# Kernel tuning notes

Hardware: AMD Instinct MI355X
Metric: run time of the kernel (lower is better)

## Reference

```python
import jax, jax.numpy as jnp
import numpy as np

N = 128       # n_channels
B = 131072    # batch
C = np.float32(np.sqrt(0.5))  # 50/50 beamsplitter amplitude (c = s = sqrt(0.5))


def setup_inputs() -> dict:
    key = jax.random.key(0)
    k1, k2, k3, k4 = jax.random.split(key, 4)
    M = N * (N - 1) // 2
    return {
        "x_real": jax.random.normal(k1, (B, N), jnp.float32),
        "x_imag": jax.random.normal(k2, (B, N), jnp.float32),
        "mzi_phases": jax.random.normal(k3, (M * 2,), jnp.float32) * 0.1,
        "output_phases": jax.random.normal(k4, (N,), jnp.float32) * 0.1,
    }


def _construct_unitary(mzi_phases, output_phases):
    n = output_phases.shape[0]
    m = n * (n - 1) // 2
    # pair ordering matches the torch double loop: i ascending, then j > i (row-major triu)
    i_np, j_np = np.triu_indices(n, 1)
    i_idx = jnp.asarray(i_np, jnp.int32)
    j_idx = jnp.asarray(j_np, jnp.int32)
    ph = mzi_phases.reshape(m, 2)
    theta, phi = ph[:, 0], ph[:, 1]

    def step(U, xs):
        th, ph_, i, j = xs
        e_phi = jax.lax.complex(jnp.cos(ph_), jnp.sin(ph_))
        e_th = jax.lax.complex(jnp.cos(th), jnp.sin(th))
        ri = U[i]
        rj = U[j]
        # T_ij @ U touches only rows i and j (O(N) Givens row update)
        new_i = C * ri + (C * e_phi) * rj
        new_j = (C * e_th) * ri - (C * e_th * e_phi) * rj
        U = U.at[i].set(new_i).at[j].set(new_j)
        return U, None

    def chunk_body(U, xs_chunk):
        U, _ = jax.lax.scan(step, U, xs_chunk)
        return U, None

    # chunk the M sequential updates: M = (n-1) * (n//2) for even n;
    # checkpointing chunks keeps reverse-mode memory O(sqrt-ish) instead of O(M * N^2)
    n_chunks = n - 1
    cs = n // 2
    xs = (theta.reshape(n_chunks, cs), phi.reshape(n_chunks, cs),
          i_idx.reshape(n_chunks, cs), j_idx.reshape(n_chunks, cs))
    U0 = jnp.eye(n, dtype=jnp.complex64)
    U, _ = jax.lax.scan(jax.checkpoint(chunk_body), U0, xs)
    # output phase screen D @ U
    d = jax.lax.complex(jnp.cos(output_phases), jnp.sin(output_phases))
    return d[:, None] * U


def reference(x_real, x_imag, mzi_phases, output_phases):
    U = _construct_unitary(mzi_phases, output_phases)           # [N, N] complex64
    x = jax.lax.complex(x_real, x_imag)                          # [B, N] complex64
    # matmul(U, x.unsqueeze(-1)).squeeze(-1) == x @ U^T
    out = jnp.einsum('nm,bm->bn', U, x)                          # [B, N] complex64
    # ComplexDropout is identity in eval mode
    return out
```

## Files before the change

kernel.cpp:

```cpp
#include <hip/hip_runtime.h>
#include <hip/hip_bf16.h>

#define NDIM 128
#define N2   (NDIM * NDIM)
#define BDIM 131072
#define NMZI 8128
#define NCHUNK 16
#define NJG 8
#define NCOL 32
#define NLOC 16
static constexpr float CC = 0.70710678118654752440f;

typedef __attribute__((ext_vector_type(8))) short bf16x8;
typedef __attribute__((ext_vector_type(4))) float f32x4;

__device__ __align__(16) float2         g_V[NCHUNK * N2];
__device__ __align__(16) float2         g_W[4 * N2];
__device__ __align__(16) unsigned short g_TB[32 * NDIM * 8];
__device__ __align__(16) unsigned short g_Ur[16 * NDIM * 8];
__device__ __align__(16) unsigned short g_Ui[16 * NDIM * 8];

__device__ inline unsigned short f2bf(float f) {
    union { __hip_bfloat16 h; unsigned short u; } cv;
    cv.h = __float2bfloat16(f);
    return cv.u;
}

#define CFMA(acc, av, b)                                                    \
    acc.x = fmaf(av.x, b.x, fmaf(-av.y, b.y, acc.x));                       \
    acc.y = fmaf(av.x, b.y, fmaf( av.y, b.x, acc.y));

__global__ __launch_bounds__(256) void build_scan(const float* __restrict__ mzi) {
    __shared__ float2 Usm[NDIM][NCOL];
    __shared__ float4 ph[2][NDIM];
    __shared__ float4 cmp[NJG][NCOL];
    const int tid   = threadIdx.x;
    const int c     = tid & 31;
    const int g     = tid >> 5;
    const int col0  = blockIdx.x * NCOL;
    const int chunk = blockIdx.y;
    const int i0    = chunk * 8;
    const int iEnd  = min(i0 + 8, NDIM - 1);
    const int nsw   = iEnd - i0;

    for (int k = g; k < NDIM; k += NJG)
        Usm[k][c] = make_float2((k == col0 + c) ? 1.f : 0.f, 0.f);

    const float2* mzp = (const float2*)mzi;
    int base = 127 * i0 - (i0 * (i0 - 1)) / 2;
    {
        const int L0 = NDIM - 1 - i0;
        if (tid < L0) {
            const float2 mz = mzp[base + tid];
            float sp, cp, st, ct;
            sincosf(mz.y, &sp, &cp);
            sincosf(mz.x, &st, &ct);
            ph[0][tid] = make_float4(cp, sp, CC * ct, CC * st);
        }
    }
    __syncthreads();

    #pragma unroll 1
    for (int sw = 0; sw < nsw; ++sw) {
        const int i = i0 + sw;
        const int L = NDIM - 1 - i;
        const int cur = sw & 1;

        float2 mznext;
        const bool have = (sw < nsw - 1) && (tid < L - 1);
        if (have) mznext = mzp[base + L + tid];

        const float2 r0 = Usm[i][c];
        const int nloc  = (L + NJG - 1) >> 3;
        const int myBeg = g * nloc;
        const int myN   = max(0, min(nloc, L - myBeg));

        float2 treg[NLOC];
        float2 qth[NLOC];
        float  A = 1.f;
        float2 Bc = make_float2(0.f, 0.f);
        #pragma unroll
        for (int kk = 0; kk < NLOC; ++kk) {
            if (kk < myN) {
                const int off = myBeg + kk;
                const float4 q  = ph[cur][off];
                const float2 rj = Usm[i + 1 + off][c];
                const float tr = fmaf(q.x, rj.x, -q.y * rj.y);
                const float ti = fmaf(q.x, rj.y,  q.y * rj.x);
                treg[kk] = make_float2(tr, ti);
                qth[kk]  = make_float2(q.z, q.w);
                Bc.x = CC * (Bc.x + tr);
                Bc.y = CC * (Bc.y + ti);
                A *= CC;
            }
        }
        cmp[g][c] = make_float4(A, Bc.x, Bc.y, 0.f);
        __syncthreads();

        float2 r = r0;
        for (int h2 = 0; h2 < g; ++h2) {
            const float4 cm = cmp[h2][c];
            r.x = fmaf(cm.x, r.x, cm.y);
            r.y = fmaf(cm.x, r.y, cm.z);
        }

        #pragma unroll
        for (int kk = 0; kk < NLOC; ++kk) {
            if (kk < myN) {
                const float2 t = treg[kk];
                const float2 q = qth[kk];
                const float dr = r.x - t.x, di = r.y - t.y;
                const float njx = fmaf(q.x, dr, -q.y * di);
                const float njy = fmaf(q.x, di,  q.y * dr);
                Usm[i + 1 + myBeg + kk][c] = make_float2(njx, njy);
                r.x = CC * (r.x + t.x);
                r.y = CC * (r.y + t.y);
            }
        }
        if (myN > 0 && (myBeg + myN == L))
            Usm[i][c] = r;

        if (have) {
            float sp, cp, st, ct;
            sincosf(mznext.y, &sp, &cp);
            sincosf(mznext.x, &st, &ct);
            ph[cur ^ 1][tid] = make_float4(cp, sp, CC * ct, CC * st);
        }
        __syncthreads();
        base += L;
    }

    float2* Vp = g_V + chunk * N2;
    for (int k = g; k < NDIM; k += NJG)
        Vp[k * NDIM + col0 + c] = Usm[k][c];
}

__global__ __launch_bounds__(256) void compose_quad() {
    __shared__ float2 As[4 * NDIM];
    __shared__ float2 part[2][4][NDIM];
    const int tid = threadIdx.x;
    const int h   = tid >> 7;
    const int m   = tid & 127;
    const int gq  = blockIdx.y;
    const int n0  = blockIdx.x * 4;

    if (h == 0) {
        const float2* A = g_V + (4 * gq + 3) * N2;
        #pragma unroll
        for (int r = 0; r < 4; ++r) As[r * NDIM + m] = A[(n0 + r) * NDIM + m];
    }
    __syncthreads();

    #pragma unroll 1
    for (int step = 2; step >= 0; --step) {
        const float2* B = g_V + (4 * gq + step) * N2;
        const int kbase = h * 64;
        float2 a0 = {0.f, 0.f}, a1 = {0.f, 0.f}, a2 = {0.f, 0.f}, a3 = {0.f, 0.f};
        float2 bb[8];
        #pragma unroll
        for (int u = 0; u < 8; ++u) bb[u] = B[(kbase + u) * NDIM + m];
        #pragma unroll 1
        for (int k0 = 0; k0 < 64; k0 += 8) {
            #pragma unroll
            for (int u = 0; u < 8; ++u) {
                const float2 bv = bb[u];
                bb[u] = B[(kbase + k0 + 8 + u) * NDIM + m];
                const int k = kbase + k0 + u;
                float2 av;
                av = As[0 * NDIM + k]; CFMA(a0, av, bv)
                av = As[1 * NDIM + k]; CFMA(a1, av, bv)
                av = As[2 * NDIM + k]; CFMA(a2, av, bv)
                av = As[3 * NDIM + k]; CFMA(a3, av, bv)
            }
        }
        part[h][0][m] = a0; part[h][1][m] = a1;
        part[h][2][m] = a2; part[h][3][m] = a3;
        __syncthreads();
        if (h == 0) {
            #pragma unroll
            for (int r = 0; r < 4; ++r) {
                const float2 p0 = part[0][r][m], p1 = part[1][r][m];
                const float2 s = make_float2(p0.x + p1.x, p0.y + p1.y);
                if (step > 0) As[r * NDIM + m] = s;
                else          g_W[gq * N2 + (n0 + r) * NDIM + m] = s;
            }
        }
        __syncthreads();
    }
}

__global__ __launch_bounds__(256) void compose_final4(const float* __restrict__ oph) {
    __shared__ float2 As[4 * NDIM];
    __shared__ float2 part[2][4][NDIM];
    const int tid = threadIdx.x;
    const int h   = tid >> 7;
    const int m   = tid & 127;
    const int n0  = blockIdx.x * 4;

    if (h == 0) {
        const float2* A = g_W + 3 * N2;
        #pragma unroll
        for (int r = 0; r < 4; ++r) As[r * NDIM + m] = A[(n0 + r) * NDIM + m];
    }
    __syncthreads();

    #pragma unroll 1
    for (int step = 2; step >= 0; --step) {
        const float2* B = g_W + step * N2;
        const int kbase = h * 64;
        float2 a0 = {0.f, 0.f}, a1 = {0.f, 0.f}, a2 = {0.f, 0.f}, a3 = {0.f, 0.f};
        float2 bb[8];
        #pragma unroll
        for (int u = 0; u < 8; ++u) bb[u] = B[(kbase + u) * NDIM + m];
        #pragma unroll 1
        for (int k0 = 0; k0 < 64; k0 += 8) {
            #pragma unroll
            for (int u = 0; u < 8; ++u) {
                const float2 bv = bb[u];
                bb[u] = B[(kbase + k0 + 8 + u) * NDIM + m];
                const int k = kbase + k0 + u;
                float2 av;
                av = As[0 * NDIM + k]; CFMA(a0, av, bv)
                av = As[1 * NDIM + k]; CFMA(a1, av, bv)
                av = As[2 * NDIM + k]; CFMA(a2, av, bv)
                av = As[3 * NDIM + k]; CFMA(a3, av, bv)
            }
        }
        part[h][0][m] = a0; part[h][1][m] = a1;
        part[h][2][m] = a2; part[h][3][m] = a3;
        __syncthreads();
        if (h == 0) {
            if (step > 0) {
                #pragma unroll
                for (int r = 0; r < 4; ++r) {
                    const float2 p0 = part[0][r][m], p1 = part[1][r][m];
                    As[r * NDIM + m] = make_float2(p0.x + p1.x, p0.y + p1.y);
                }
            } else {
                const int kg = m >> 3, e = m & 7;
                #pragma unroll
                for (int r = 0; r < 4; ++r) {
                    const float2 p0 = part[0][r][m], p1 = part[1][r][m];
                    const float2 u = make_float2(p0.x + p1.x, p0.y + p1.y);
                    const int n = n0 + r;
                    float ds, dc;
                    sincosf(oph[n], &ds, &dc);
                    const float vr = fmaf(u.x, dc, -u.y * ds);
                    const float vi = fmaf(u.x, ds,  u.y * dc);
                    g_TB[(kg * NDIM + n) * 8 + e]        = f2bf(vr);
                    g_TB[((16 + kg) * NDIM + n) * 8 + e] = f2bf(-vi);
                    g_Ur[(kg * NDIM + n) * 8 + e] = f2bf(vr);
                    g_Ui[(kg * NDIM + n) * 8 + e] = f2bf(vi);
                }
            }
        }
        __syncthreads();
    }
}

__global__ __launch_bounds__(256) void cmatmul0(const float* __restrict__ xr,
                                                const float* __restrict__ xi,
                                                float* __restrict__ out) {
    __shared__ __align__(16) char smX[4][8192];
    const int tid  = threadIdx.x;
    const int lane = tid & 63;
    const int w    = tid >> 6;
    const int r15  = lane & 15;
    const int kg4  = lane >> 4;
    const int l31  = lane & 31;
    const int lh   = lane >> 5;
    const int R    = blockIdx.x * 64 + w * 16;

    const f32x4* sre = (const f32x4*)(xr + (size_t)R * NDIM);
    const f32x4* sim = (const f32x4*)(xi + (size_t)R * NDIM);
    f32x4 G[16];
    #pragma unroll
    for (int p = 0; p < 8; ++p) G[p]     = __builtin_nontemporal_load(sre + p * 64 + lane);
    #pragma unroll
    for (int p = 0; p < 8; ++p) G[8 + p] = __builtin_nontemporal_load(sim + p * 64 + lane);

    char* buf = &smX[w][0];
    #pragma unroll
    for (int p = 0; p < 8; ++p) {
        const int row = 2 * p + lh;
        const int swz = (row & 7) << 4;
        uint2 v;
        v.x = ((unsigned)f2bf(G[p][1]) << 16) | f2bf(G[p][0]);
        v.y = ((unsigned)f2bf(G[p][3]) << 16) | f2bf(G[p][2]);
        *(uint2*)(buf + row * 512 + ((l31 * 8) ^ swz)) = v;
        v.x = ((unsigned)f2bf(G[8 + p][1]) << 16) | f2bf(G[8 + p][0]);
        v.y = ((unsigned)f2bf(G[8 + p][3]) << 16) | f2bf(G[8 + p][2]);
        *(uint2*)(buf + row * 512 + 256 + ((l31 * 8) ^ swz)) = v;
    }

    bf16x8 fx[8];
    const int rswz = (r15 & 7) << 4;
    #pragma unroll
    for (int kc = 0; kc < 8; ++kc) {
        const int off = (((kc & 3) * 64 + kg4 * 16) ^ rswz) + ((kc >= 4) ? 256 : 0);
        fx[kc] = *(const bf16x8*)(buf + r15 * 512 + off);
    }

    const bf16x8* gT = (const bf16x8*)g_TB;
    #pragma unroll
    for (int nt = 0; nt < 8; ++nt) {
        f32x4 a0 = {0.f, 0.f, 0.f, 0.f};
        f32x4 a1 = {0.f, 0.f, 0.f, 0.f};
        #pragma unroll
        for (int kc = 0; kc < 4; ++kc)
            a0 = __builtin_amdgcn_mfma_f32_16x16x32_bf16(
                gT[(kc * 4 + kg4) * NDIM + nt * 16 + r15], fx[kc], a0, 0, 0, 0);
        #pragma unroll
        for (int kc = 4; kc < 8; ++kc)
            a1 = __builtin_amdgcn_mfma_f32_16x16x32_bf16(
                gT[(kc * 4 + kg4) * NDIM + nt * 16 + r15], fx[kc], a1, 0, 0, 0);
        const f32x4 s = a0 + a1;
        *(f32x4*)(buf + r15 * 512 + ((nt * 64 + kg4 * 16) ^ rswz)) = s;
    }

    char* outp = (char*)(out + (size_t)R * NDIM);
    #pragma unroll
    for (int p = 0; p < 8; ++p) {
        const int bofs = p * 1024 + lane * 16;
        const int row  = bofs >> 9;
        const int colb = bofs & 511;
        const f32x4 v = *(const f32x4*)(buf + row * 512 + (colb ^ ((row & 7) << 4)));
        __builtin_nontemporal_store(v, (f32x4*)(outp + bofs));
    }
}

__global__ __launch_bounds__(256) void cmatmul1(const float* __restrict__ xr,
                                                const float* __restrict__ xi,
                                                ushort2* __restrict__ outp) {
    const int lane  = threadIdx.x & 63;
    const int w     = threadIdx.x >> 6;
    const int btile = blockIdx.x * 64 + w * 16;
    const int r15   = lane & 15;
    const int kg4   = lane >> 4;
    const int bload = btile + r15;

    const bf16x8* Ur = (const bf16x8*)g_Ur;
    const bf16x8* Ui = (const bf16x8*)g_Ui;
    const float* xrp = xr + (size_t)bload * NDIM;
    const float* xip = xi + (size_t)bload * NDIM;

    bf16x8 ar[4], ai[4], ain[4];
    #pragma unroll
    for (int kc = 0; kc < 4; ++kc) {
        const int k0 = kc * 32 + kg4 * 8;
        float4 rlo = *(const float4*)(xrp + k0);
        float4 rhi = *(const float4*)(xrp + k0 + 4);
        float4 ilo = *(const float4*)(xip + k0);
        float4 ihi = *(const float4*)(xip + k0 + 4);
        bf16x8 vr, vi, vn;
        vr[0] = (short)f2bf(rlo.x); vr[1] = (short)f2bf(rlo.y);
        vr[2] = (short)f2bf(rlo.z); vr[3] = (short)f2bf(rlo.w);
        vr[4] = (short)f2bf(rhi.x); vr[5] = (short)f2bf(rhi.y);
        vr[6] = (short)f2bf(rhi.z); vr[7] = (short)f2bf(rhi.w);
        vi[0] = (short)f2bf(ilo.x); vi[1] = (short)f2bf(ilo.y);
        vi[2] = (short)f2bf(ilo.z); vi[3] = (short)f2bf(ilo.w);
        vi[4] = (short)f2bf(ihi.x); vi[5] = (short)f2bf(ihi.y);
        vi[6] = (short)f2bf(ihi.z); vi[7] = (short)f2bf(ihi.w);
        #pragma unroll
        for (int e = 0; e < 8; ++e) vn[e] = (short)(vi[e] ^ 0x8000);
        ar[kc] = vr; ai[kc] = vi; ain[kc] = vn;
    }

    #pragma unroll
    for (int nt = 0; nt < 8; ++nt) {
        f32x4 accR = {0.f, 0.f, 0.f, 0.f};
        f32x4 accI = {0.f, 0.f, 0.f, 0.f};
        #pragma unroll
        for (int kc = 0; kc < 4; ++kc) {
            const int kg = kc * 4 + kg4;
            bf16x8 br = Ur[kg * NDIM + nt * 16 + r15];
            bf16x8 bi = Ui[kg * NDIM + nt * 16 + r15];
            accR = __builtin_amdgcn_mfma_f32_16x16x32_bf16(ar[kc],  br, accR, 0, 0, 0);
            accR = __builtin_amdgcn_mfma_f32_16x16x32_bf16(ain[kc], bi, accR, 0, 0, 0);
            accI = __builtin_amdgcn_mfma_f32_16x16x32_bf16(ar[kc],  bi, accI, 0, 0, 0);
            accI = __builtin_amdgcn_mfma_f32_16x16x32_bf16(ai[kc],  br, accI, 0, 0, 0);
        }
        const int n    = nt * 16 + r15;
        const int brow = btile + kg4 * 4;
        #pragma unroll
        for (int r = 0; r < 4; ++r)
            outp[(size_t)(brow + r) * NDIM + n] = make_ushort2(f2bf(accR[r]), f2bf(accI[r]));
    }
}

extern "C" void kernel_launch(void* const* d_in, const int* in_sizes, int n_in,
                              void* d_out, int out_size, void* d_ws, size_t ws_size,
                              hipStream_t stream) {
    const float* xr  = (const float*)d_in[0];
    const float* xi  = (const float*)d_in[1];
    const float* mzi = (const float*)d_in[2];
    const float* oph = (const float*)d_in[3];

    build_scan<<<dim3(4, NCHUNK), dim3(256), 0, stream>>>(mzi);
    compose_quad<<<dim3(32, 4), dim3(256), 0, stream>>>();
    compose_final4<<<dim3(32), dim3(256), 0, stream>>>(oph);
    if (out_size == BDIM * NDIM) {
        cmatmul0<<<dim3(BDIM / 64), dim3(256), 0, stream>>>(xr, xi, (float*)d_out);
    } else {
        cmatmul1<<<dim3(BDIM / 64), dim3(256), 0, stream>>>(xr, xi, (ushort2*)d_out);
    }
}
```

Before: 110.4 us.

## Fuse unitary build and compose kernels into one persistent kernel with grid barriers

Merges the three small build/compose kernels into one 128-block kernel, separated by atomic-counter grid barriers. The aim is to remove two kernel launch gaps from the critical path. The counters are reset at the start of the following matmul kernel, so correctness relies on all 128 blocks being co-resident and on that reset running before the next call. Blocks that have no scan work now sit idle waiting at the barrier.

```diff
diff --git a/kernel.cpp b/kernel.cpp
--- a/kernel.cpp
+++ b/kernel.cpp
@@ -6,6 +6,7 @@
 #define BDIM 131072
 #define NMZI 8128
 #define NCHUNK 16
+#define NBLK 128
 #define NJG 8
 #define NCOL 32
 #define NLOC 16
@@ -19,6 +20,7 @@
 __device__ __align__(16) unsigned short g_TB[32 * NDIM * 8];
 __device__ __align__(16) unsigned short g_Ur[16 * NDIM * 8];
 __device__ __align__(16) unsigned short g_Ui[16 * NDIM * 8];
+__device__ unsigned g_ctr[3];
 
 __device__ inline unsigned short f2bf(float f) {
     union { __hip_bfloat16 h; unsigned short u; } cv;
@@ -26,241 +28,271 @@
     return cv.u;
 }
 
+__device__ __forceinline__ void gbar(int idx) {
+    __syncthreads();
+    asm volatile("" ::: "memory");
+    if (threadIdx.x == 0) {
+        __threadfence();
+        __hip_atomic_fetch_add(&g_ctr[idx], 1u, __ATOMIC_RELEASE, __HIP_MEMORY_SCOPE_AGENT);
+        while (__hip_atomic_load(&g_ctr[idx], __ATOMIC_RELAXED, __HIP_MEMORY_SCOPE_AGENT)
+               < (unsigned)NBLK)
+            __builtin_amdgcn_s_sleep(2);
+        __threadfence();
+    }
+    __syncthreads();
+    asm volatile("" ::: "memory");
+}
+
 #define CFMA(acc, av, b)                                                    \
     acc.x = fmaf(av.x, b.x, fmaf(-av.y, b.y, acc.x));                       \
     acc.y = fmaf(av.x, b.y, fmaf( av.y, b.x, acc.y));
 
-__global__ __launch_bounds__(256) void build_scan(const float* __restrict__ mzi) {
-    __shared__ float2 Usm[NDIM][NCOL];
-    __shared__ float4 ph[2][NDIM];
-    __shared__ float4 cmp[NJG][NCOL];
-    const int tid   = threadIdx.x;
-    const int c     = tid & 31;
-    const int g     = tid >> 5;
-    const int col0  = blockIdx.x * NCOL;
-    const int chunk = blockIdx.y;
-    const int i0    = chunk * 8;
-    const int iEnd  = min(i0 + 8, NDIM - 1);
-    const int nsw   = iEnd - i0;
-
-    for (int k = g; k < NDIM; k += NJG)
-        Usm[k][c] = make_float2((k == col0 + c) ? 1.f : 0.f, 0.f);
-
-    const float2* mzp = (const float2*)mzi;
-    int base = 127 * i0 - (i0 * (i0 - 1)) / 2;
+__global__ __launch_bounds__(256) void build_all(const float* __restrict__ mzi,
+                                                 const float* __restrict__ oph) {
+    __shared__ __align__(16) char SM[40960];
+    const int tid = threadIdx.x;
+    const int b   = blockIdx.x;
+
+    if (b < 64) {
+        float2 (*Usm)[NCOL] = reinterpret_cast<float2(*)[NCOL]>(SM);
+        float4 (*ph)[NDIM]  = reinterpret_cast<float4(*)[NDIM]>(SM + 32768);
+        float4 (*cmp)[NCOL] = reinterpret_cast<float4(*)[NCOL]>(SM + 36864);
+        const int c     = tid & 31;
+        const int g     = tid >> 5;
+        const int col0  = (b & 3) * NCOL;
+        const int chunk = b >> 2;
+        const int i0    = chunk * 8;
+        const int iEnd  = min(i0 + 8, NDIM - 1);
+        const int nsw   = iEnd - i0;
+
+        for (int k = g; k < NDIM; k += NJG)
+            Usm[k][c] = make_float2((k == col0 + c) ? 1.f : 0.f, 0.f);
+
+        const float2* mzp = (const float2*)mzi;
+        int base = 127 * i0 - (i0 * (i0 - 1)) / 2;
+        {
+            const int L0 = NDIM - 1 - i0;
+            if (tid < L0) {
+                const float2 mz = mzp[base + tid];
+                float sp, cp, st, ct;
+                sincosf(mz.y, &sp, &cp);
+                sincosf(mz.x, &st, &ct);
+                ph[0][tid] = make_float4(cp, sp, CC * ct, CC * st);
+            }
+        }
+        __syncthreads();
+
+        #pragma unroll 1
+        for (int sw = 0; sw < nsw; ++sw) {
+            const int i = i0 + sw;
+            const int L = NDIM - 1 - i;
+            const int cur = sw & 1;
+
+            float2 mznext;
+            const bool have = (sw < nsw - 1) && (tid < L - 1);
+            if (have) mznext = mzp[base + L + tid];
+
+            const float2 r0 = Usm[i][c];
+            const int nloc  = (L + NJG - 1) >> 3;
+            const int myBeg = g * nloc;
+            const int myN   = max(0, min(nloc, L - myBeg));
+
+            float2 treg[NLOC];
+            float2 qth[NLOC];
+            float  A = 1.f;
+            float2 Bc = make_float2(0.f, 0.f);
+            #pragma unroll
+            for (int kk = 0; kk < NLOC; ++kk) {
+                if (kk < myN) {
+                    const int off = myBeg + kk;
+                    const float4 q  = ph[cur][off];
+                    const float2 rj = Usm[i + 1 + off][c];
+                    const float tr = fmaf(q.x, rj.x, -q.y * rj.y);
+                    const float ti = fmaf(q.x, rj.y,  q.y * rj.x);
+                    treg[kk] = make_float2(tr, ti);
+                    qth[kk]  = make_float2(q.z, q.w);
+                    Bc.x = CC * (Bc.x + tr);
+                    Bc.y = CC * (Bc.y + ti);
+                    A *= CC;
+                }
+            }
+            cmp[g][c] = make_float4(A, Bc.x, Bc.y, 0.f);
+            __syncthreads();
+
+            float2 r = r0;
+            for (int h2 = 0; h2 < g; ++h2) {
+                const float4 cm = cmp[h2][c];
+                r.x = fmaf(cm.x, r.x, cm.y);
+                r.y = fmaf(cm.x, r.y, cm.z);
+            }
+
+            #pragma unroll
+            for (int kk = 0; kk < NLOC; ++kk) {
+                if (kk < myN) {
+                    const float2 t = treg[kk];
+                    const float2 q = qth[kk];
+                    const float dr = r.x - t.x, di = r.y - t.y;
+                    const float njx = fmaf(q.x, dr, -q.y * di);
+                    const float njy = fmaf(q.x, di,  q.y * dr);
+                    Usm[i + 1 + myBeg + kk][c] = make_float2(njx, njy);
+                    r.x = CC * (r.x + t.x);
+                    r.y = CC * (r.y + t.y);
+                }
+            }
+            if (myN > 0 && (myBeg + myN == L))
+                Usm[i][c] = r;
+
+            if (have) {
+                float sp, cp, st, ct;
+                sincosf(mznext.y, &sp, &cp);
+                sincosf(mznext.x, &st, &ct);
+                ph[cur ^ 1][tid] = make_float4(cp, sp, CC * ct, CC * st);
+            }
+            __syncthreads();
+            base += L;
+        }
+
+        float2* Vp = g_V + chunk * N2;
+        for (int k = g; k < NDIM; k += NJG)
+            Vp[k * NDIM + col0 + c] = Usm[k][c];
+    }
+
+    gbar(0);
+
     {
-        const int L0 = NDIM - 1 - i0;
-        if (tid < L0) {
-            const float2 mz = mzp[base + tid];
-            float sp, cp, st, ct;
-            sincosf(mz.y, &sp, &cp);
-            sincosf(mz.x, &st, &ct);
-            ph[0][tid] = make_float4(cp, sp, CC * ct, CC * st);
-        }
-    }
-    __syncthreads();
-
-    #pragma unroll 1
-    for (int sw = 0; sw < nsw; ++sw) {
-        const int i = i0 + sw;
-        const int L = NDIM - 1 - i;
-        const int cur = sw & 1;
-
-        float2 mznext;
-        const bool have = (sw < nsw - 1) && (tid < L - 1);
-        if (have) mznext = mzp[base + L + tid];
-
-        const float2 r0 = Usm[i][c];
-        const int nloc  = (L + NJG - 1) >> 3;
-        const int myBeg = g * nloc;
-        const int myN   = max(0, min(nloc, L - myBeg));
-
-        float2 treg[NLOC];
-        float2 qth[NLOC];
-        float  A = 1.f;
-        float2 Bc = make_float2(0.f, 0.f);
-        #pragma unroll
-        for (int kk = 0; kk < NLOC; ++kk) {
-            if (kk < myN) {
-                const int off = myBeg + kk;
-                const float4 q  = ph[cur][off];
-                const float2 rj = Usm[i + 1 + off][c];
-                const float tr = fmaf(q.x, rj.x, -q.y * rj.y);
-                const float ti = fmaf(q.x, rj.y,  q.y * rj.x);
-                treg[kk] = make_float2(tr, ti);
-                qth[kk]  = make_float2(q.z, q.w);
-                Bc.x = CC * (Bc.x + tr);
-                Bc.y = CC * (Bc.y + ti);
-                A *= CC;
-            }
-        }
-        cmp[g][c] = make_float4(A, Bc.x, Bc.y, 0.f);
+        float2* As = (float2*)SM;
+        float2 (*part)[4][NDIM] =
+            reinterpret_cast<float2(*)[4][NDIM]>(SM + 4096);
+        const int h  = tid >> 7;
+        const int m  = tid & 127;
+        const int gq = b >> 5;
+        const int n0 = (b & 31) * 4;
+
+        if (h == 0) {
+            const float2* A = g_V + (4 * gq + 3) * N2;
+            #pragma unroll
+            for (int r = 0; r < 4; ++r) As[r * NDIM + m] = A[(n0 + r) * NDIM + m];
+        }
         __syncthreads();
 
-        float2 r = r0;
-        for (int h2 = 0; h2 < g; ++h2) {
-            const float4 cm = cmp[h2][c];
-            r.x = fmaf(cm.x, r.x, cm.y);
-            r.y = fmaf(cm.x, r.y, cm.z);
-        }
-
-        #pragma unroll
-        for (int kk = 0; kk < NLOC; ++kk) {
-            if (kk < myN) {
-                const float2 t = treg[kk];
-                const float2 q = qth[kk];
-                const float dr = r.x - t.x, di = r.y - t.y;
-                const float njx = fmaf(q.x, dr, -q.y * di);
-                const float njy = fmaf(q.x, di,  q.y * dr);
-                Usm[i + 1 + myBeg + kk][c] = make_float2(njx, njy);
-                r.x = CC * (r.x + t.x);
-                r.y = CC * (r.y + t.y);
-            }
-        }
-        if (myN > 0 && (myBeg + myN == L))
-            Usm[i][c] = r;
-
-        if (have) {
-            float sp, cp, st, ct;
-            sincosf(mznext.y, &sp, &cp);
-            sincosf(mznext.x, &st, &ct);
-            ph[cur ^ 1][tid] = make_float4(cp, sp, CC * ct, CC * st);
-        }
-        __syncthreads();
-        base += L;
-    }
-
-    float2* Vp = g_V + chunk * N2;
-    for (int k = g; k < NDIM; k += NJG)
-        Vp[k * NDIM + col0 + c] = Usm[k][c];
-}
-
-__global__ __launch_bounds__(256) void compose_quad() {
-    __shared__ float2 As[4 * NDIM];
-    __shared__ float2 part[2][4][NDIM];
-    const int tid = threadIdx.x;
-    const int h   = tid >> 7;
-    const int m   = tid & 127;
-    const int gq  = blockIdx.y;
-    const int n0  = blockIdx.x * 4;
-
-    if (h == 0) {
-        const float2* A = g_V + (4 * gq + 3) * N2;
-        #pragma unroll
-        for (int r = 0; r < 4; ++r) As[r * NDIM + m] = A[(n0 + r) * NDIM + m];
-    }
-    __syncthreads();
-
-    #pragma unroll 1
-    for (int step = 2; step >= 0; --step) {
-        const float2* B = g_V + (4 * gq + step) * N2;
-        const int kbase = h * 64;
-        float2 a0 = {0.f, 0.f}, a1 = {0.f, 0.f}, a2 = {0.f, 0.f}, a3 = {0.f, 0.f};
-        float2 bb[8];
-        #pragma unroll
-        for (int u = 0; u < 8; ++u) bb[u] = B[(kbase + u) * NDIM + m];
         #pragma unroll 1
-        for (int k0 = 0; k0 < 64; k0 += 8) {
-            #pragma unroll
-            for (int u = 0; u < 8; ++u) {
-                const float2 bv = bb[u];
-                bb[u] = B[(kbase + k0 + 8 + u) * NDIM + m];
-                const int k = kbase + k0 + u;
-                float2 av;
-                av = As[0 * NDIM + k]; CFMA(a0, av, bv)
-                av = As[1 * NDIM + k]; CFMA(a1, av, bv)
-                av = As[2 * NDIM + k]; CFMA(a2, av, bv)
-                av = As[3 * NDIM + k]; CFMA(a3, av, bv)
-            }
-        }
-        part[h][0][m] = a0; part[h][1][m] = a1;
-        part[h][2][m] = a2; part[h][3][m] = a3;
-        __syncthreads();
-        if (h == 0) {
-            #pragma unroll
-            for (int r = 0; r < 4; ++r) {
-                const float2 p0 = part[0][r][m], p1 = part[1][r][m];
-                const float2 s = make_float2(p0.x + p1.x, p0.y + p1.y);
-                if (step > 0) As[r * NDIM + m] = s;
-                else          g_W[gq * N2 + (n0 + r) * NDIM + m] = s;
-            }
-        }
-        __syncthreads();
-    }
-}
-
-__global__ __launch_bounds__(256) void compose_final4(const float* __restrict__ oph) {
-    __shared__ float2 As[4 * NDIM];
-    __shared__ float2 part[2][4][NDIM];
-    const int tid = threadIdx.x;
-    const int h   = tid >> 7;
-    const int m   = tid & 127;
-    const int n0  = blockIdx.x * 4;
-
-    if (h == 0) {
-        const float2* A = g_W + 3 * N2;
-        #pragma unroll
-        for (int r = 0; r < 4; ++r) As[r * NDIM + m] = A[(n0 + r) * NDIM + m];
-    }
-    __syncthreads();
-
-    #pragma unroll 1
-    for (int step = 2; step >= 0; --step) {
-        const float2* B = g_W + step * N2;
-        const int kbase = h * 64;
-        float2 a0 = {0.f, 0.f}, a1 = {0.f, 0.f}, a2 = {0.f, 0.f}, a3 = {0.f, 0.f};
-        float2 bb[8];
-        #pragma unroll
-        for (int u = 0; u < 8; ++u) bb[u] = B[(kbase + u) * NDIM + m];
-        #pragma unroll 1
-        for (int k0 = 0; k0 < 64; k0 += 8) {
-            #pragma unroll
-            for (int u = 0; u < 8; ++u) {
-                const float2 bv = bb[u];
-                bb[u] = B[(kbase + k0 + 8 + u) * NDIM + m];
-                const int k = kbase + k0 + u;
-                float2 av;
-                av = As[0 * NDIM + k]; CFMA(a0, av, bv)
-                av = As[1 * NDIM + k]; CFMA(a1, av, bv)
-                av = As[2 * NDIM + k]; CFMA(a2, av, bv)
-                av = As[3 * NDIM + k]; CFMA(a3, av, bv)
-            }
-        }
-        part[h][0][m] = a0; part[h][1][m] = a1;
-        part[h][2][m] = a2; part[h][3][m] = a3;
-        __syncthreads();
-        if (h == 0) {
-            if (step > 0) {
+        for (int step = 2; step >= 0; --step) {
+            const float2* B = g_V + (4 * gq + step) * N2;
+            const int kbase = h * 64;
+            float2 a0 = {0.f, 0.f}, a1 = {0.f, 0.f}, a2 = {0.f, 0.f}, a3 = {0.f, 0.f};
+            float2 bb[8];
+            #pragma unroll
+            for (int u = 0; u < 8; ++u) bb[u] = B[(kbase + u) * NDIM + m];
+            #pragma unroll 1
+            for (int k0 = 0; k0 < 64; k0 += 8) {
+                #pragma unroll
+                for (int u = 0; u < 8; ++u) {
+                    const float2 bv = bb[u];
+                    bb[u] = B[(kbase + k0 + 8 + u) * NDIM + m];
+                    const int k = kbase + k0 + u;
+                    float2 av;
+                    av = As[0 * NDIM + k]; CFMA(a0, av, bv)
+                    av = As[1 * NDIM + k]; CFMA(a1, av, bv)
+                    av = As[2 * NDIM + k]; CFMA(a2, av, bv)
+                    av = As[3 * NDIM + k]; CFMA(a3, av, bv)
+                }
+            }
+            part[h][0][m] = a0; part[h][1][m] = a1;
+            part[h][2][m] = a2; part[h][3][m] = a3;
+            __syncthreads();
+            if (h == 0) {
                 #pragma unroll
                 for (int r = 0; r < 4; ++r) {
                     const float2 p0 = part[0][r][m], p1 = part[1][r][m];
-                    As[r * NDIM + m] = make_float2(p0.x + p1.x, p0.y + p1.y);
-                }
-            } else {
-                const int kg = m >> 3, e = m & 7;
+                    const float2 s = make_float2(p0.x + p1.x, p0.y + p1.y);
+                    if (step > 0) As[r * NDIM + m] = s;
+                    else          g_W[gq * N2 + (n0 + r) * NDIM + m] = s;
+                }
+            }
+            __syncthreads();
+        }
+    }
+
+    gbar(1);
+
+    if (b < 32) {
+        float2* As = (float2*)SM;
+        float2 (*part)[4][NDIM] =
+            reinterpret_cast<float2(*)[4][NDIM]>(SM + 4096);
+        const int h  = tid >> 7;
+        const int m  = tid & 127;
+        const int n0 = b * 4;
+
+        if (h == 0) {
+            const float2* A = g_W + 3 * N2;
+            #pragma unroll
+            for (int r = 0; r < 4; ++r) As[r * NDIM + m] = A[(n0 + r) * NDIM + m];
+        }
+        __syncthreads();
+
+        #pragma unroll 1
+        for (int step = 2; step >= 0; --step) {
+            const float2* B = g_W + step * N2;
+            const int kbase = h * 64;
+            float2 a0 = {0.f, 0.f}, a1 = {0.f, 0.f}, a2 = {0.f, 0.f}, a3 = {0.f, 0.f};
+            float2 bb[8];
+            #pragma unroll
+            for (int u = 0; u < 8; ++u) bb[u] = B[(kbase + u) * NDIM + m];
+            #pragma unroll 1
+            for (int k0 = 0; k0 < 64; k0 += 8) {
                 #pragma unroll
-                for (int r = 0; r < 4; ++r) {
-                    const float2 p0 = part[0][r][m], p1 = part[1][r][m];
-                    const float2 u = make_float2(p0.x + p1.x, p0.y + p1.y);
-                    const int n = n0 + r;
-                    float ds, dc;
-                    sincosf(oph[n], &ds, &dc);
-                    const float vr = fmaf(u.x, dc, -u.y * ds);
-                    const float vi = fmaf(u.x, ds,  u.y * dc);
-                    g_TB[(kg * NDIM + n) * 8 + e]        = f2bf(vr);
-                    g_TB[((16 + kg) * NDIM + n) * 8 + e] = f2bf(-vi);
-                    g_Ur[(kg * NDIM + n) * 8 + e] = f2bf(vr);
-                    g_Ui[(kg * NDIM + n) * 8 + e] = f2bf(vi);
-                }
-            }
-        }
-        __syncthreads();
+                for (int u = 0; u < 8; ++u) {
+                    const float2 bv = bb[u];
+                    bb[u] = B[(kbase + k0 + 8 + u) * NDIM + m];
+                    const int k = kbase + k0 + u;
+                    float2 av;
+                    av = As[0 * NDIM + k]; CFMA(a0, av, bv)
+                    av = As[1 * NDIM + k]; CFMA(a1, av, bv)
+                    av = As[2 * NDIM + k]; CFMA(a2, av, bv)
+                    av = As[3 * NDIM + k]; CFMA(a3, av, bv)
+                }
+            }
+            part[h][0][m] = a0; part[h][1][m] = a1;
+            part[h][2][m] = a2; part[h][3][m] = a3;
+            __syncthreads();
+            if (h == 0) {
+                if (step > 0) {
+                    #pragma unroll
+                    for (int r = 0; r < 4; ++r) {
+                        const float2 p0 = part[0][r][m], p1 = part[1][r][m];
+                        As[r * NDIM + m] = make_float2(p0.x + p1.x, p0.y + p1.y);
+                    }
+                } else {
+                    const int kg = m >> 3, e = m & 7;
+                    #pragma unroll
+                    for (int r = 0; r < 4; ++r) {
+                        const float2 p0 = part[0][r][m], p1 = part[1][r][m];
+                        const float2 u = make_float2(p0.x + p1.x, p0.y + p1.y);
+                        const int n = n0 + r;
+                        float ds, dc;
+                        sincosf(oph[n], &ds, &dc);
+                        const float vr = fmaf(u.x, dc, -u.y * ds);
+                        const float vi = fmaf(u.x, ds,  u.y * dc);
+                        g_TB[(kg * NDIM + n) * 8 + e]        = f2bf(vr);
+                        g_TB[((16 + kg) * NDIM + n) * 8 + e] = f2bf(-vi);
+                        g_Ur[(kg * NDIM + n) * 8 + e] = f2bf(vr);
+                        g_Ui[(kg * NDIM + n) * 8 + e] = f2bf(vi);
+                    }
+                }
+            }
+            __syncthreads();
+        }
     }
 }
 
 __global__ __launch_bounds__(256) void cmatmul0(const float* __restrict__ xr,
                                                 const float* __restrict__ xi,
                                                 float* __restrict__ out) {
+    if (blockIdx.x == 0 && threadIdx.x == 0) {
+        #pragma unroll
+        for (int i = 0; i < 3; ++i)
+            __hip_atomic_store(&g_ctr[i], 0u, __ATOMIC_RELAXED, __HIP_MEMORY_SCOPE_AGENT);
+    }
     __shared__ __align__(16) char smX[4][8192];
     const int tid  = threadIdx.x;
     const int lane = tid & 63;
@@ -332,6 +364,11 @@
 __global__ __launch_bounds__(256) void cmatmul1(const float* __restrict__ xr,
                                                 const float* __restrict__ xi,
                                                 ushort2* __restrict__ outp) {
+    if (blockIdx.x == 0 && threadIdx.x == 0) {
+        #pragma unroll
+        for (int i = 0; i < 3; ++i)
+            __hip_atomic_store(&g_ctr[i], 0u, __ATOMIC_RELAXED, __HIP_MEMORY_SCOPE_AGENT);
+    }
     const int lane  = threadIdx.x & 63;
     const int w     = threadIdx.x >> 6;
     const int btile = blockIdx.x * 64 + w * 16;
@@ -396,9 +433,7 @@
     const float* mzi = (const float*)d_in[2];
     const float* oph = (const float*)d_in[3];
 
-    build_scan<<<dim3(4, NCHUNK), dim3(256), 0, stream>>>(mzi);
-    compose_quad<<<dim3(32, 4), dim3(256), 0, stream>>>();
-    compose_final4<<<dim3(32), dim3(256), 0, stream>>>(oph);
+    build_all<<<dim3(NBLK), dim3(256), 0, stream>>>(mzi, oph);
     if (out_size == BDIM * NDIM) {
         cmatmul0<<<dim3(BDIM / 64), dim3(256), 0, stream>>>(xr, xi, (float*)d_out);
     } else {
```

Result: no change. 111.9 us (+1.4%).
